# Performance work log

Hardware: AMD Instinct MI355X
Metric: run time of the kernel (lower is better)

Reference implementation:

```python
import jax, jax.numpy as jnp
import numpy as np

NG, NPG, EPG = 64, 256, 2048        # graphs, nodes/graph, edges/graph
N, E = NG * NPG, NG * EPG
FN, FE, FG = 256, 64, 128           # node/edge/global feature dims
MSG_DIMS = [FE + 2 * FN + FG, 512, 512, 256]   # message_arch '512-512-256'
UPD_DIMS = [256 + FN + FG, 512, 256]           # node_arch '512-256'
N_EMB_G, OUT_NODE, OUT_ACT = 256, 64, 8


def _mlp(x, params):
    # Linear -> ReLU stack (Dropout is identity in eval mode)
    for w, b in params:
        x = jax.nn.relu(x @ w + b)
    return x


def setup_inputs():
    key = jax.random.key(0)
    ks = jax.random.split(key, 24)
    nodes = jax.random.normal(ks[0], (N, FN), jnp.float32)
    edge_attr = jax.random.normal(ks[1], (E, FE), jnp.float32)
    global_attr = jax.random.normal(ks[2], (NG, FG), jnp.float32)
    # edges are grouped by graph (matches repeat_interleave(global, num_edges))
    rng = np.random.default_rng(0)
    gid_e = np.repeat(np.arange(NG), EPG)
    src = gid_e * NPG + rng.integers(0, NPG, E)
    tgt = gid_e * NPG + rng.integers(0, NPG, E)
    edge_indices = jnp.asarray(np.stack([src, tgt]), jnp.int32)
    num_nodes = jnp.full((NG,), NPG, jnp.int32)
    num_edges = jnp.full((NG,), EPG, jnp.int32)
    batch_indices = jnp.asarray(np.repeat(np.arange(NG), NPG), jnp.int32)

    def lin(k, fi, fo):
        kw, kb = jax.random.split(k)
        lim = 1.0 / np.sqrt(fi)
        return (jax.random.uniform(kw, (fi, fo), jnp.float32, -lim, lim),
                jax.random.uniform(kb, (fo,), jnp.float32, -lim, lim))

    inp = dict(nodes=nodes, edge_attr=edge_attr, global_attr=global_attr,
               edge_indices=edge_indices, num_nodes=num_nodes,
               num_edges=num_edges, batch_indices=batch_indices)
    for i in range(3):
        w, b = lin(ks[3 + i], MSG_DIMS[i], MSG_DIMS[i + 1])
        inp[f'msg_w{i}'], inp[f'msg_b{i}'] = w, b
    for i in range(2):
        w, b = lin(ks[6 + i], UPD_DIMS[i], UPD_DIMS[i + 1])
        inp[f'upd_w{i}'], inp[f'upd_b{i}'] = w, b
    inp['glob_w'], inp['glob_b'] = lin(ks[8], UPD_DIMS[-1] + FG, N_EMB_G)
    inp['emb_w'], inp['emb_b'] = lin(ks[9], UPD_DIMS[-1], OUT_NODE)
    inp['act_w'], inp['act_b'] = lin(ks[10], N_EMB_G, OUT_ACT)
    return inp


def reference(nodes, edge_attr, global_attr, edge_indices, num_nodes,
              num_edges, batch_indices, msg_w0, msg_b0, msg_w1, msg_b1,
              msg_w2, msg_b2, upd_w0, upd_b0, upd_w1, upd_b1,
              glob_w, glob_b, emb_w, emb_b, act_w, act_b):
    n, e = nodes.shape[0], edge_indices.shape[1]
    ng = global_attr.shape[0]
    src, tgt = edge_indices[0], edge_indices[1]
    glob_e = jnp.repeat(global_attr, num_edges, axis=0, total_repeat_length=e)
    concat = jnp.concatenate([nodes[src], edge_attr, nodes[tgt], glob_e], axis=1)
    # message_nn ends with ReLU; outer F.relu is a no-op on non-neg values
    message = _mlp(concat, [(msg_w0, msg_b0), (msg_w1, msg_b1), (msg_w2, msg_b2)])
    # scatter_max into per-node slots; messages >= 0 so zeros init matches fill=0
    aggr = jnp.zeros((n, message.shape[1]), message.dtype).at[tgt].max(message)
    glob_n = jnp.repeat(global_attr, num_nodes, axis=0, total_repeat_length=n)
    h = _mlp(jnp.concatenate([nodes, aggr, glob_n], axis=1),
             [(upd_w0, upd_b0), (upd_w1, upd_b1)])
    agg_nodes = jnp.zeros((ng, h.shape[1]), h.dtype).at[batch_indices].max(h)
    g = jax.nn.relu(jnp.concatenate([agg_nodes, global_attr], axis=1) @ glob_w + glob_b)
    node_pred = jax.nn.relu(h @ emb_w + emb_b)
    action = jax.nn.softmax(g @ act_w + act_b, axis=1)
    return node_pred, action
```

## Files before the change

### kernel.cpp

```cpp
#include <hip/hip_runtime.h>
#include <hip/hip_bf16.h>

typedef unsigned short u16;
using u16x4 = __attribute__((ext_vector_type(4))) unsigned short;
using u16x8 = __attribute__((ext_vector_type(8))) unsigned short;
using u32x4 = __attribute__((ext_vector_type(4))) unsigned int;
using f32x4 = __attribute__((ext_vector_type(4))) float;
using bf16x8 = __attribute__((ext_vector_type(8))) __bf16;

#define TNG 64
#define TNN 16384
#define TNE 131072
#define TFN 256
#define TFE 64
#define TFG 128

__device__ __forceinline__ u16 f2bf(float f) {
    unsigned u = __float_as_uint(f);
    unsigned r = (u + 0x7FFFu + ((u >> 16) & 1u)) >> 16;
    return (u16)r;
}
__device__ __forceinline__ float b2f(u16 h) {
    return __uint_as_float(((unsigned)h) << 16);
}

__device__ __forceinline__ void gload_lds16(const u16* g, u16* l) {
    __builtin_amdgcn_global_load_lds(
        (const __attribute__((address_space(1))) void*)g,
        (__attribute__((address_space(3))) void*)l, 16, 0, 0);
}

__device__ __forceinline__ int xcd_swz(int bid, int nwg) {
    return (nwg & 7) == 0 ? (bid & 7) * (nwg >> 3) + (bid >> 3) : bid;
}


__global__ void cast_kernel(const float* __restrict__ in, u16* __restrict__ out, int n4) {
    int i = blockIdx.x * 256 + threadIdx.x;
    if (i >= n4) return;
    f32x4 v = *(const f32x4*)(in + (size_t)i * 4);
    u16x4 o;
    o.x = f2bf(v.x); o.y = f2bf(v.y); o.z = f2bf(v.z); o.w = f2bf(v.w);
    *(u16x4*)(out + (size_t)i * 4) = o;
}


struct PrepTab {
    const float* W[8];
    int out_off[8];
    int Nin[8], Nact[8], r0[8], Ksub[8];
    int tile0[8];
    int tkn[8];
};

__global__ __launch_bounds__(256) void prep_weights_kernel(PrepTab tab, u16* __restrict__ wsbase) {
    const int b = blockIdx.x;
    int i = 7;
#pragma unroll
    for (int j = 7; j > 0; --j)
        if (b < tab.tile0[j]) i = j - 1;
    const int loc = b - tab.tile0[i];
    const int tk = loc % tab.tkn[i];
    const int tn = loc / tab.tkn[i];
    const int kb = tk * 64, nb = tn * 64;
    const int Nin = tab.Nin[i], Nact = tab.Nact[i], r0 = tab.r0[i], Ksub = tab.Ksub[i];
    const float* W = tab.W[i];
    u16* outp = wsbase + tab.out_off[i];

    __shared__ float t[64][65];
    const int tid = threadIdx.x;
    const int nl = tid & 63;
    const bool nok = (nb + nl) < Nact;
#pragma unroll 4
    for (int kk = tid >> 6; kk < 64; kk += 4) {
        float v = nok ? W[(size_t)(r0 + kb + kk) * Nin + nb + nl] : 0.0f;
        t[kk][nl] = v;
    }
    __syncthreads();
    const int kl = tid & 63;
#pragma unroll 4
    for (int nn = tid >> 6; nn < 64; nn += 4)
        outp[(size_t)(nb + nn) * Ksub + kb + kl] = f2bf(t[kl][nn]);
}


template <int K, int NXSH, bool RELU, bool OUT_BF16>
__global__ __launch_bounds__(256) void gemm_bt_kernel(
    const u16* __restrict__ A, const u16* __restrict__ Bt,
    const float* __restrict__ bias, void* __restrict__ Cv,
    int Nout, int ldc) {
    constexpr int NT = K / 32;
    __shared__ u16 As[3][4096];
    __shared__ u16 Bs[3][4096];
    const int w = xcd_swz(blockIdx.x, gridDim.x);
    const int bxi = w & ((1 << NXSH) - 1);
    const int byi = w >> NXSH;
    const int tid = threadIdx.x;
    const int wave = tid >> 6, lane = tid & 63;
    const int wr = wave >> 1, wc = wave & 1;
    const size_t brow = (size_t)byi * 128;
    const size_t bcol = (size_t)bxi * 128;
    const int srow = tid >> 2;
    const int qsrc = (tid & 3) ^ ((srow >> 1) & 3);
    const u16* aSrc = A + (brow + srow) * (size_t)K + qsrc * 8;
    const u16* bSrc = Bt + (bcol + srow) * (size_t)K + qsrc * 8;
    const size_t stepRows = (size_t)64 * K;

    auto stage = [&](int t, int buf) {
        const int k0 = t * 32;
        gload_lds16(aSrc + k0, &As[buf][tid * 8]);
        gload_lds16(aSrc + stepRows + k0, &As[buf][tid * 8 + 2048]);
        gload_lds16(bSrc + k0, &Bs[buf][tid * 8]);
        gload_lds16(bSrc + stepRows + k0, &Bs[buf][tid * 8 + 2048]);
    };

    f32x4 acc[4][4] = {};

    stage(0, 0);
    stage(1, 1);
#pragma unroll
    for (int t = 0; t < NT; ++t) {
        const int cur = t % 3;
        if (t + 1 < NT) asm volatile("s_waitcnt vmcnt(4)" ::: "memory");
        else            asm volatile("s_waitcnt vmcnt(0)" ::: "memory");
        __builtin_amdgcn_s_barrier();
        if (t + 2 < NT) stage(t + 2, (t + 2) % 3);
        bf16x8 af[4], bfv[4];
#pragma unroll
        for (int m = 0; m < 4; ++m) {
            const int row = wr * 64 + m * 16 + (lane & 15);
            const int slot = (lane >> 4) ^ ((row >> 1) & 3);
            af[m] = *(const bf16x8*)&As[cur][row * 32 + slot * 8];
        }
#pragma unroll
        for (int n = 0; n < 4; ++n) {
            const int row = wc * 64 + n * 16 + (lane & 15);
            const int slot = (lane >> 4) ^ ((row >> 1) & 3);
            bfv[n] = *(const bf16x8*)&Bs[cur][row * 32 + slot * 8];
        }
#pragma unroll
        for (int m = 0; m < 4; ++m)
#pragma unroll
            for (int n = 0; n < 4; ++n)
                acc[m][n] = __builtin_amdgcn_mfma_f32_16x16x32_bf16(af[m], bfv[n], acc[m][n], 0, 0, 0);
    }

    const int rowSub = wr * 64 + (lane >> 4) * 4;
#pragma unroll
    for (int n = 0; n < 4; ++n) {
        const int col = (int)bcol + wc * 64 + n * 16 + (lane & 15);
        if (col >= Nout) continue;
        const float bv = bias ? bias[col] : 0.0f;
#pragma unroll
        for (int m = 0; m < 4; ++m) {
#pragma unroll
            for (int i = 0; i < 4; ++i) {
                float v = acc[m][n][i] + bv;
                if (RELU) v = fmaxf(v, 0.0f);
                size_t off = (brow + rowSub + m * 16 + i) * (size_t)ldc + col;
                if (OUT_BF16) ((u16*)Cv)[off] = f2bf(v);
                else ((float*)Cv)[off] = v;
            }
        }
    }
}


__global__ __launch_bounds__(256) void gemm_u0_kernel(
    const u16* __restrict__ nodes_bf, const u16* __restrict__ aggr,
    const u16* __restrict__ glob_bf, const u16* __restrict__ U0T,
    const float* __restrict__ bias, u16* __restrict__ C) {
    constexpr int NT = 20;
    __shared__ u16 As[3][4096];
    __shared__ u16 Bs[3][4096];
    const int w = xcd_swz(blockIdx.x, gridDim.x);
    const int bxi = w & 3;
    const int byi = w >> 2;
    const int tid = threadIdx.x;
    const int wave = tid >> 6, lane = tid & 63;
    const int wr = wave >> 1, wc = wave & 1;
    const size_t brow = (size_t)byi * 128;
    const size_t bcol = (size_t)bxi * 128;
    const int srow = tid >> 2;
    const int scol = ((tid & 3) ^ ((srow >> 1) & 3)) * 8;
    const int r0i = (int)brow + srow;
    const u16* bSrc = U0T + (bcol + srow) * (size_t)640 + scol;

    auto stage = [&](int t, int buf) {
        const int k0 = t * 32;
        const u16 *p0, *p1;
        if (k0 < 256) {
            p0 = nodes_bf + (size_t)r0i * 256 + k0 + scol;
            p1 = nodes_bf + (size_t)(r0i + 64) * 256 + k0 + scol;
        } else if (k0 < 512) {
            p0 = aggr + (size_t)r0i * 256 + (k0 - 256) + scol;
            p1 = aggr + (size_t)(r0i + 64) * 256 + (k0 - 256) + scol;
        } else {
            p0 = glob_bf + (size_t)(r0i >> 8) * 128 + (k0 - 512) + scol;
            p1 = glob_bf + (size_t)((r0i + 64) >> 8) * 128 + (k0 - 512) + scol;
        }
        gload_lds16(p0, &As[buf][tid * 8]);
        gload_lds16(p1, &As[buf][tid * 8 + 2048]);
        gload_lds16(bSrc + k0, &Bs[buf][tid * 8]);
        gload_lds16(bSrc + (size_t)64 * 640 + k0, &Bs[buf][tid * 8 + 2048]);
    };

    f32x4 acc[4][4] = {};

    stage(0, 0);
    stage(1, 1);
#pragma unroll
    for (int t = 0; t < NT; ++t) {
        const int cur = t % 3;
        if (t + 1 < NT) asm volatile("s_waitcnt vmcnt(4)" ::: "memory");
        else            asm volatile("s_waitcnt vmcnt(0)" ::: "memory");
        __builtin_amdgcn_s_barrier();
        if (t + 2 < NT) stage(t + 2, (t + 2) % 3);
        bf16x8 af[4], bfv[4];
#pragma unroll
        for (int m = 0; m < 4; ++m) {
            const int row = wr * 64 + m * 16 + (lane & 15);
            const int slot = (lane >> 4) ^ ((row >> 1) & 3);
            af[m] = *(const bf16x8*)&As[cur][row * 32 + slot * 8];
        }
#pragma unroll
        for (int n = 0; n < 4; ++n) {
            const int row = wc * 64 + n * 16 + (lane & 15);
            const int slot = (lane >> 4) ^ ((row >> 1) & 3);
            bfv[n] = *(const bf16x8*)&Bs[cur][row * 32 + slot * 8];
        }
#pragma unroll
        for (int m = 0; m < 4; ++m)
#pragma unroll
            for (int n = 0; n < 4; ++n)
                acc[m][n] = __builtin_amdgcn_mfma_f32_16x16x32_bf16(af[m], bfv[n], acc[m][n], 0, 0, 0);
    }

    const int rowSub = wr * 64 + (lane >> 4) * 4;
#pragma unroll
    for (int n = 0; n < 4; ++n) {
        const int col = (int)bcol + wc * 64 + n * 16 + (lane & 15);
        const float bv = bias[col];
#pragma unroll
        for (int m = 0; m < 4; ++m)
#pragma unroll
            for (int i = 0; i < 4; ++i) {
                float v = fmaxf(acc[m][n][i] + bv, 0.0f);
                C[(brow + rowSub + m * 16 + i) * (size_t)512 + col] = f2bf(v);
            }
    }
}


__global__ __launch_bounds__(256) void gd_kernel(const float* __restrict__ glob,
                                                 const float* __restrict__ msg_w0,
                                                 const float* __restrict__ b0,
                                                 float* __restrict__ Gdb,
                                                 u16* __restrict__ glob_bf) {
    int g = blockIdx.x;
    __shared__ float in[TFG];
    if (threadIdx.x < TFG) {
        float v = glob[g * TFG + threadIdx.x];
        in[threadIdx.x] = v;
        glob_bf[g * TFG + threadIdx.x] = f2bf(v);
    }
    __syncthreads();
    for (int j = threadIdx.x; j < 512; j += 256) {
        float s = b0[j];
        for (int k = 0; k < TFG; ++k) s += in[k] * msg_w0[(size_t)(576 + k) * 512 + j];
        Gdb[(size_t)g * 512 + j] = s;
    }
}


__global__ __launch_bounds__(256) void h1_fused_kernel(
    const float* __restrict__ Ef, const u16* __restrict__ WbT,
    const u16* __restrict__ Pac, const float* __restrict__ Gdb,
    const int* __restrict__ src, const int* __restrict__ tgt,
    u16* __restrict__ h1, int e0) {
    __shared__ u16 smem[17408];
    u16* As = smem;
    u16* Bs = smem + 8192;
    const int w = xcd_swz(blockIdx.x, gridDim.x);
    const int bxi = w & 3;
    const int byi = w >> 2;
    const int tid = threadIdx.x;
    const int wave = tid >> 6, lane = tid & 63;
    const int wr = wave >> 1, wc = wave & 1;
    const int brow = byi * 128;
    const int bcol = bxi * 128;

    {
        const int r = tid >> 2;
        const int cq = (tid & 3) * 2;
        const int sw = r & 7;
#pragma unroll
        for (int h = 0; h < 2; ++h) {
            const float* sp = Ef + (size_t)(e0 + brow + r + h * 64) * 64 + cq * 8;
            f32x4 v0 = *(const f32x4*)(sp);
            f32x4 v1 = *(const f32x4*)(sp + 4);
            f32x4 v2 = *(const f32x4*)(sp + 8);
            f32x4 v3 = *(const f32x4*)(sp + 12);
            u16x8 o0, o1;
            o0[0] = f2bf(v0.x); o0[1] = f2bf(v0.y); o0[2] = f2bf(v0.z); o0[3] = f2bf(v0.w);
            o0[4] = f2bf(v1.x); o0[5] = f2bf(v1.y); o0[6] = f2bf(v1.z); o0[7] = f2bf(v1.w);
            o1[0] = f2bf(v2.x); o1[1] = f2bf(v2.y); o1[2] = f2bf(v2.z); o1[3] = f2bf(v2.w);
            o1[4] = f2bf(v3.x); o1[5] = f2bf(v3.y); o1[6] = f2bf(v3.z); o1[7] = f2bf(v3.w);
            *(u16x8*)&As[(r + h * 64) * 64 + (cq ^ sw) * 8] = o0;
            *(u16x8*)&As[(r + h * 64) * 64 + ((cq + 1) ^ sw) * 8] = o1;
        }
#pragma unroll
        for (int j = 0; j < 4; ++j) {
            int li = j * 256 + tid;
            int row = li >> 3;
            int gslot = (li & 7) ^ (row & 7);
            gload_lds16(WbT + (size_t)(bcol + row) * 64 + gslot * 8, &Bs[li * 8]);
        }
    }
    __syncthreads();

    f32x4 acc[4][4] = {};
#pragma unroll
    for (int k0 = 0; k0 < 64; k0 += 32) {
        bf16x8 af[4], bv[4];
#pragma unroll
        for (int m = 0; m < 4; ++m) {
            const int row = wr * 64 + m * 16 + (lane & 15);
            const int slot = ((k0 >> 3) + (lane >> 4)) ^ (row & 7);
            af[m] = *(const bf16x8*)&As[row * 64 + slot * 8];
        }
#pragma unroll
        for (int n = 0; n < 4; ++n) {
            const int row = wc * 64 + n * 16 + (lane & 15);
            const int slot = ((k0 >> 3) + (lane >> 4)) ^ (row & 7);
            bv[n] = *(const bf16x8*)&Bs[row * 64 + slot * 8];
        }
#pragma unroll
        for (int m = 0; m < 4; ++m)
#pragma unroll
            for (int n = 0; n < 4; ++n)
                acc[m][n] = __builtin_amdgcn_mfma_f32_16x16x32_bf16(af[m], bv[n], acc[m][n], 0, 0, 0);
    }
    __syncthreads();

    const int rowSub = wr * 64 + (lane >> 4) * 4;
#pragma unroll
    for (int m = 0; m < 4; ++m)
#pragma unroll
        for (int n = 0; n < 4; ++n)
#pragma unroll
            for (int i = 0; i < 4; ++i)
                smem[(rowSub + m * 16 + i) * 136 + wc * 64 + n * 16 + (lane & 15)] =
                    f2bf(acc[m][n][i]);
    __syncthreads();

#pragma unroll
    for (int it = 0; it < 8; ++it) {
        int lin = it * 256 + tid;
        int r = lin >> 4;
        int q = (lin & 15) * 8;
        int e = e0 + brow + r;
        int s = src[e];
        int t = tgt[e];
        int g = e >> 11;
        int col = bcol + q;
        u16x8 pa = *(const u16x8*)(Pac + (size_t)s * 1024 + col);
        u16x8 pc = *(const u16x8*)(Pac + (size_t)t * 1024 + 512 + col);
        u16x8 eb = *(const u16x8*)&smem[r * 136 + q];
        f32x4 g0 = *(const f32x4*)(Gdb + (size_t)g * 512 + col);
        f32x4 g1 = *(const f32x4*)(Gdb + (size_t)g * 512 + col + 4);
        u16x8 o;
#pragma unroll
        for (int j = 0; j < 8; ++j) {
            float gd = (j < 4) ? g0[j] : g1[j - 4];
            float v = b2f(pa[j]) + b2f(pc[j]) + b2f(eb[j]) + gd;
            o[j] = f2bf(fmaxf(v, 0.0f));
        }
        *(u16x8*)(h1 + (size_t)(brow + r) * 512 + col) = o;
    }
}


__global__ __launch_bounds__(1024) void scatter_max_kernel(
    const u16* __restrict__ msg, const int* __restrict__ tgt,
    u16* __restrict__ aggr, int g0, int e0) {
    int g = g0 + (blockIdx.x >> 2);
    int fc = blockIdx.x & 3;
    __shared__ unsigned smax[256 * 64];
    int tid = threadIdx.x;
    for (int i = tid; i < 256 * 64; i += 1024) smax[i] = 0u;
    __syncthreads();
    const int eg = g * 2048;
    const int n0 = g * 256;
    const int f4 = (tid & 15) * 4;
    const int elane = tid >> 4;
    const u16* mbase = msg + fc * 64 + f4;
#pragma unroll
    for (int wv = 0; wv < 32; wv += 4) {
        const int e = eg + elane + wv * 64;
        int t0 = tgt[e], t1 = tgt[e + 64], t2 = tgt[e + 128], t3 = tgt[e + 192];
        u16x4 m0 = *(const u16x4*)(mbase + (size_t)(e       - e0) * 256);
        u16x4 m1 = *(const u16x4*)(mbase + (size_t)(e +  64 - e0) * 256);
        u16x4 m2 = *(const u16x4*)(mbase + (size_t)(e + 128 - e0) * 256);
        u16x4 m3 = *(const u16x4*)(mbase + (size_t)(e + 192 - e0) * 256);
        int a0 = t0 - n0, a1 = t1 - n0, a2 = t2 - n0, a3 = t3 - n0;
        if ((unsigned)a0 < 256u) {
            atomicMax(&smax[a0 * 64 + f4],     ((unsigned)m0.x) << 16);
            atomicMax(&smax[a0 * 64 + f4 + 1], ((unsigned)m0.y) << 16);
            atomicMax(&smax[a0 * 64 + f4 + 2], ((unsigned)m0.z) << 16);
            atomicMax(&smax[a0 * 64 + f4 + 3], ((unsigned)m0.w) << 16);
        }
        if ((unsigned)a1 < 256u) {
            atomicMax(&smax[a1 * 64 + f4],     ((unsigned)m1.x) << 16);
            atomicMax(&smax[a1 * 64 + f4 + 1], ((unsigned)m1.y) << 16);
            atomicMax(&smax[a1 * 64 + f4 + 2], ((unsigned)m1.z) << 16);
            atomicMax(&smax[a1 * 64 + f4 + 3], ((unsigned)m1.w) << 16);
        }
        if ((unsigned)a2 < 256u) {
            atomicMax(&smax[a2 * 64 + f4],     ((unsigned)m2.x) << 16);
            atomicMax(&smax[a2 * 64 + f4 + 1], ((unsigned)m2.y) << 16);
            atomicMax(&smax[a2 * 64 + f4 + 2], ((unsigned)m2.z) << 16);
            atomicMax(&smax[a2 * 64 + f4 + 3], ((unsigned)m2.w) << 16);
        }
        if ((unsigned)a3 < 256u) {
            atomicMax(&smax[a3 * 64 + f4],     ((unsigned)m3.x) << 16);
            atomicMax(&smax[a3 * 64 + f4 + 1], ((unsigned)m3.y) << 16);
            atomicMax(&smax[a3 * 64 + f4 + 2], ((unsigned)m3.z) << 16);
            atomicMax(&smax[a3 * 64 + f4 + 3], ((unsigned)m3.w) << 16);
        }
    }
    __syncthreads();
    for (int i = tid; i < 256 * 64; i += 1024) {
        int nl = i >> 6, ff = i & 63;
        aggr[(size_t)(n0 + nl) * 256 + fc * 64 + ff] = (u16)(smax[nl * 64 + ff] >> 16);
    }
}


__global__ __launch_bounds__(256) void head_kernel(
    const u16* __restrict__ h, const float* __restrict__ glob,
    const float* __restrict__ W, const float* __restrict__ b,
    const float* __restrict__ actw, const float* __restrict__ actb,
    float* __restrict__ out_act) {
    int g = blockIdx.x;
    int tid = threadIdx.x;
    __shared__ float in[384];
    __shared__ float go[256];
    __shared__ float logits[8];
    {
        const size_t base = (size_t)g * 256 * 256 + tid;
        float m0 = 0.0f, m1 = 0.0f, m2 = 0.0f, m3 = 0.0f;
        for (int n = 0; n < 256; n += 4) {
            m0 = fmaxf(m0, b2f(h[base + (size_t)n * 256]));
            m1 = fmaxf(m1, b2f(h[base + (size_t)(n + 1) * 256]));
            m2 = fmaxf(m2, b2f(h[base + (size_t)(n + 2) * 256]));
            m3 = fmaxf(m3, b2f(h[base + (size_t)(n + 3) * 256]));
        }
        in[tid] = fmaxf(fmaxf(m0, m1), fmaxf(m2, m3));
        if (tid < 128) in[256 + tid] = glob[(size_t)g * 128 + tid];
    }
    __syncthreads();
    {
        float s = b[tid];
        for (int k = 0; k < 384; ++k) s += in[k] * W[(size_t)k * 256 + tid];
        go[tid] = fmaxf(s, 0.0f);
    }
    __syncthreads();
    if (tid < 8) {
        float s = actb[tid];
        for (int k = 0; k < 256; ++k) s += go[k] * actw[(size_t)k * 8 + tid];
        logits[tid] = s;
    }
    __syncthreads();
    if (tid == 0) {
        float mx = logits[0];
        for (int i = 1; i < 8; ++i) mx = fmaxf(mx, logits[i]);
        float ex[8], den = 0.0f;
        for (int i = 0; i < 8; ++i) { ex[i] = expf(logits[i] - mx); den += ex[i]; }
        float inv = 1.0f / den;
        for (int i = 0; i < 8; ++i) out_act[(size_t)g * 8 + i] = ex[i] * inv;
    }
}


constexpr size_t OFF_NODES_BF = 0;
constexpr size_t OFF_GLOB_BF  = OFF_NODES_BF + (size_t)TNN * TFN * 2;
constexpr size_t OFF_WACT = OFF_GLOB_BF + (size_t)TNG * TFG * 2;
constexpr size_t OFF_WBT  = OFF_WACT + 1024 * 256 * 2;
constexpr size_t OFF_W1T  = OFF_WBT + 512 * 64 * 2;
constexpr size_t OFF_W2T  = OFF_W1T + 512 * 512 * 2;
constexpr size_t OFF_U0T  = OFF_W2T + 256 * 512 * 2;
constexpr size_t OFF_U1T  = OFF_U0T + 512 * 640 * 2;
constexpr size_t OFF_EMBT = OFF_U1T + 256 * 512 * 2;
constexpr size_t OFF_AGGR = OFF_EMBT + 128 * 256 * 2;
constexpr size_t OFF_GDB  = OFF_AGGR + (size_t)TNN * 256 * 2;
constexpr size_t OFF_PAC  = OFF_GDB + 64 * 512 * 4;
constexpr size_t OFF_V    = OFF_PAC + (size_t)TNN * 1024 * 2;
constexpr size_t SZ_HU1   = (size_t)TNN * 512 * 2;

extern "C" void kernel_launch(void* const* d_in, const int* in_sizes, int n_in,
                              void* d_out, int out_size, void* d_ws, size_t ws_size,
                              hipStream_t stream) {
    const float* nodes       = (const float*)d_in[0];
    const float* edge_attr   = (const float*)d_in[1];
    const float* global_attr = (const float*)d_in[2];
    const int*   edge_idx    = (const int*)d_in[3];
    const float* msg_w0 = (const float*)d_in[7];
    const float* msg_b0 = (const float*)d_in[8];
    const float* msg_w1 = (const float*)d_in[9];
    const float* msg_b1 = (const float*)d_in[10];
    const float* msg_w2 = (const float*)d_in[11];
    const float* msg_b2 = (const float*)d_in[12];
    const float* upd_w0 = (const float*)d_in[13];
    const float* upd_b0 = (const float*)d_in[14];
    const float* upd_w1 = (const float*)d_in[15];
    const float* upd_b1 = (const float*)d_in[16];
    const float* glob_w = (const float*)d_in[17];
    const float* glob_b = (const float*)d_in[18];
    const float* emb_w  = (const float*)d_in[19];
    const float* emb_b  = (const float*)d_in[20];
    const float* act_w  = (const float*)d_in[21];
    const float* act_b  = (const float*)d_in[22];

    const int* src = edge_idx;
    const int* tgt = edge_idx + TNE;

    char* ws = (char*)d_ws;
    u16* nodes_bf = (u16*)(ws + OFF_NODES_BF);
    u16* glob_bf  = (u16*)(ws + OFF_GLOB_BF);
    u16* WacT = (u16*)(ws + OFF_WACT);
    u16* WbT  = (u16*)(ws + OFF_WBT);
    u16* W1T  = (u16*)(ws + OFF_W1T);
    u16* W2T  = (u16*)(ws + OFF_W2T);
    u16* U0T  = (u16*)(ws + OFF_U0T);
    u16* U1T  = (u16*)(ws + OFF_U1T);
    u16* EmbT = (u16*)(ws + OFF_EMBT);
    u16* aggr = (u16*)(ws + OFF_AGGR);
    float* Gdb = (float*)(ws + OFF_GDB);
    u16* Pac  = (u16*)(ws + OFF_PAC);
    float* out = (float*)d_out;

    size_t CH = (size_t)TNE;
    while (CH > 2048) {
        size_t need = OFF_V + (CH * 2560 > SZ_HU1 ? CH * 2560 : SZ_HU1);
        if (need <= ws_size) break;
        CH >>= 1;
    }
    const int nchunk = (int)((size_t)TNE / CH);
    const int gpc = (int)(CH / 2048);

    u16* h1c  = (u16*)(ws + OFF_V);
    u16* h2c  = (u16*)(ws + OFF_V + CH * 1024);
    u16* msgc = (u16*)(ws + OFF_V + CH * 2048);
    u16* hu1  = (u16*)(ws + OFF_V);
    u16* h_bf = (u16*)(ws + OFF_AGGR);

    cast_kernel<<<(TNN * TFN / 4 + 255) / 256, 256, 0, stream>>>(nodes, nodes_bf, TNN * TFN / 4);

    PrepTab tab;
    int ntiles = 0;
    {
        const float* Ws[8]  = {msg_w0, msg_w0, msg_w0, msg_w1, msg_w2, upd_w0, upd_w1, emb_w};
        int offs[8] = {(int)(OFF_WACT / 2), (int)(OFF_WACT / 2) + 131072, (int)(OFF_WBT / 2),
                       (int)(OFF_W1T / 2), (int)(OFF_W2T / 2), (int)(OFF_U0T / 2),
                       (int)(OFF_U1T / 2), (int)(OFF_EMBT / 2)};
        int nin[8]  = {512, 512, 512, 512, 256, 512, 256, 64};
        int nact[8] = {512, 512, 512, 512, 256, 512, 256, 64};
        int r0v[8]  = {0, 320, 256, 0, 0, 0, 0, 0};
        int ksub[8] = {256, 256, 64, 512, 512, 640, 512, 256};
        int npad[8] = {512, 512, 512, 512, 256, 512, 256, 128};
        int acc = 0;
        for (int i = 0; i < 8; ++i) {
            tab.W[i] = Ws[i]; tab.out_off[i] = offs[i]; tab.Nin[i] = nin[i];
            tab.Nact[i] = nact[i]; tab.r0[i] = r0v[i]; tab.Ksub[i] = ksub[i];
            tab.tkn[i] = ksub[i] / 64;
            tab.tile0[i] = acc;
            acc += (npad[i] / 64) * (ksub[i] / 64);
        }
        ntiles = acc;
    }
    prep_weights_kernel<<<ntiles, 256, 0, stream>>>(tab, (u16*)ws);
    gd_kernel<<<64, 256, 0, stream>>>(global_attr, msg_w0, msg_b0, Gdb, glob_bf);

    gemm_bt_kernel<256, 3, false, true><<<1024, 256, 0, stream>>>(nodes_bf, WacT, nullptr, Pac, 1024, 1024);

    for (int ci = 0; ci < nchunk; ++ci) {
        const int e0 = (int)(ci * CH);
        const int nwg = (int)(CH / 32);
        h1_fused_kernel<<<nwg, 256, 0, stream>>>(
            edge_attr, WbT, Pac, Gdb, src, tgt, h1c, e0);
        gemm_bt_kernel<512, 2, true, true><<<nwg, 256, 0, stream>>>(h1c, W1T, msg_b1, h2c, 512, 512);
        gemm_bt_kernel<512, 1, true, true><<<nwg / 2, 256, 0, stream>>>(h2c, W2T, msg_b2, msgc, 256, 256);
        scatter_max_kernel<<<gpc * 4, 1024, 0, stream>>>(msgc, tgt, aggr, ci * gpc, e0);
    }

    gemm_u0_kernel<<<512, 256, 0, stream>>>(nodes_bf, aggr, glob_bf, U0T, upd_b0, hu1);
    gemm_bt_kernel<512, 1, true, true><<<256, 256, 0, stream>>>(hu1, U1T, upd_b1, h_bf, 256, 256);

    head_kernel<<<64, 256, 0, stream>>>(h_bf, global_attr, glob_w, glob_b,
                                        act_w, act_b, out + (size_t)TNN * 64);
    gemm_bt_kernel<256, 0, true, false><<<128, 256, 0, stream>>>(h_bf, EmbT, emb_b, out, 64, 64);

    (void)in_sizes; (void)n_in; (void)out_size;
}
```

Measured before the change: 351.6 us.

## Store full message buffer and run scatter-max once after all chunks

Allocates a dedicated buffer holding messages for all edges, so each chunk's final GEMM writes into its slice and a single scatter_max launch covers all 64 graphs instead of one small launch per chunk. The chunk size is also capped at 32768 edges rather than as large as the workspace allows, which shrinks the h1/h2 intermediates to improve cache residency. This trades extra workspace (64 MB of messages) and more chunk iterations for fewer, fuller scatter launches and possibly better L2 reuse of intermediates.

```diff
diff --git a/kernel.cpp b/kernel.cpp
--- a/kernel.cpp
+++ b/kernel.cpp
@@ -383,8 +383,8 @@
 
 __global__ __launch_bounds__(1024) void scatter_max_kernel(
     const u16* __restrict__ msg, const int* __restrict__ tgt,
-    u16* __restrict__ aggr, int g0, int e0) {
-    int g = g0 + (blockIdx.x >> 2);
+    u16* __restrict__ aggr) {
+    int g = blockIdx.x >> 2;
     int fc = blockIdx.x & 3;
     __shared__ unsigned smax[256 * 64];
     int tid = threadIdx.x;
@@ -399,10 +399,10 @@
     for (int wv = 0; wv < 32; wv += 4) {
         const int e = eg + elane + wv * 64;
         int t0 = tgt[e], t1 = tgt[e + 64], t2 = tgt[e + 128], t3 = tgt[e + 192];
-        u16x4 m0 = *(const u16x4*)(mbase + (size_t)(e       - e0) * 256);
-        u16x4 m1 = *(const u16x4*)(mbase + (size_t)(e +  64 - e0) * 256);
-        u16x4 m2 = *(const u16x4*)(mbase + (size_t)(e + 128 - e0) * 256);
-        u16x4 m3 = *(const u16x4*)(mbase + (size_t)(e + 192 - e0) * 256);
+        u16x4 m0 = *(const u16x4*)(mbase + (size_t)e * 256);
+        u16x4 m1 = *(const u16x4*)(mbase + (size_t)(e + 64) * 256);
+        u16x4 m2 = *(const u16x4*)(mbase + (size_t)(e + 128) * 256);
+        u16x4 m3 = *(const u16x4*)(mbase + (size_t)(e + 192) * 256);
         int a0 = t0 - n0, a1 = t1 - n0, a2 = t2 - n0, a3 = t3 - n0;
         if ((unsigned)a0 < 256u) {
             atomicMax(&smax[a0 * 64 + f4],     ((unsigned)m0.x) << 16);
@@ -495,7 +495,8 @@
 constexpr size_t OFF_AGGR = OFF_EMBT + 128 * 256 * 2;
 constexpr size_t OFF_GDB  = OFF_AGGR + (size_t)TNN * 256 * 2;
 constexpr size_t OFF_PAC  = OFF_GDB + 64 * 512 * 4;
-constexpr size_t OFF_V    = OFF_PAC + (size_t)TNN * 1024 * 2;
+constexpr size_t OFF_MSG  = OFF_PAC + (size_t)TNN * 1024 * 2;
+constexpr size_t OFF_V    = OFF_MSG + (size_t)TNE * 256 * 2;
 constexpr size_t SZ_HU1   = (size_t)TNN * 512 * 2;
 
 extern "C" void kernel_launch(void* const* d_in, const int* in_sizes, int n_in,
@@ -538,20 +539,15 @@
     u16* aggr = (u16*)(ws + OFF_AGGR);
     float* Gdb = (float*)(ws + OFF_GDB);
     u16* Pac  = (u16*)(ws + OFF_PAC);
+    u16* msgc = (u16*)(ws + OFF_MSG);
     float* out = (float*)d_out;
 
-    size_t CH = (size_t)TNE;
-    while (CH > 2048) {
-        size_t need = OFF_V + (CH * 2560 > SZ_HU1 ? CH * 2560 : SZ_HU1);
-        if (need <= ws_size) break;
-        CH >>= 1;
-    }
+    size_t CH = 32768;
+    while (CH > 2048 && OFF_V + CH * 2048 > ws_size) CH >>= 1;
     const int nchunk = (int)((size_t)TNE / CH);
-    const int gpc = (int)(CH / 2048);
 
     u16* h1c  = (u16*)(ws + OFF_V);
     u16* h2c  = (u16*)(ws + OFF_V + CH * 1024);
-    u16* msgc = (u16*)(ws + OFF_V + CH * 2048);
     u16* hu1  = (u16*)(ws + OFF_V);
     u16* h_bf = (u16*)(ws + OFF_AGGR);
 
@@ -590,9 +586,10 @@
         h1_fused_kernel<<<nwg, 256, 0, stream>>>(
             edge_attr, WbT, Pac, Gdb, src, tgt, h1c, e0);
         gemm_bt_kernel<512, 2, true, true><<<nwg, 256, 0, stream>>>(h1c, W1T, msg_b1, h2c, 512, 512);
-        gemm_bt_kernel<512, 1, true, true><<<nwg / 2, 256, 0, stream>>>(h2c, W2T, msg_b2, msgc, 256, 256);
-        scatter_max_kernel<<<gpc * 4, 1024, 0, stream>>>(msgc, tgt, aggr, ci * gpc, e0);
-    }
+        gemm_bt_kernel<512, 1, true, true><<<nwg / 2, 256, 0, stream>>>(
+            h2c, W2T, msg_b2, msgc + (size_t)e0 * 256, 256, 256);
+    }
+    scatter_max_kernel<<<TNG * 4, 1024, 0, stream>>>(msgc, tgt, aggr);
 
     gemm_u0_kernel<<<512, 256, 0, stream>>>(nodes_bf, aggr, glob_bf, U0T, upd_b0, hu1);
     gemm_bt_kernel<512, 1, true, true><<<256, 256, 0, stream>>>(hu1, U1T, upd_b1, h_bf, 256, 256);
```

New measurement: 348.7 us. Within noise of the previous version (-0.8%).
